# Kernel tuning notes

Hardware: AMD Instinct MI355X
Metric: run time of the kernel (lower is better)

The kernel has to match this reference:

```python
import jax, jax.numpy as jnp
import numpy as np
from jax import lax

W = 65536  # wavelength batch
L = 64     # number of stacked layers
N_IN = 1.0
N_OUT = 1.45
PURITY = 0.87
CD_SCALE = 32980.0  # mdeg conversion, as in source
LN10 = 2.302585092994046


def setup_inputs() -> dict:
    key = jax.random.key(0)
    ks = jax.random.split(key, 9)
    wl = jnp.linspace(0.4, 0.8, W, dtype=jnp.float32)  # microns, matches wl_range*1e-6 usage
    thickP = jax.random.normal(ks[0], (L,), jnp.float32) * 2.0

    def u(k, lo, hi):
        return lo + (hi - lo) * jax.random.uniform(k, (W, L), jnp.float32)

    return {
        "wl": wl,
        "thickP": thickP,
        "mind": jnp.float32(20.0),   # nm
        "maxd": jnp.float32(300.0),  # nm
        "eps_c_re": u(ks[1], 1.8, 4.5),
        "eps_c_im": u(ks[2], 0.0, 0.08),
        "kappa_c_re": u(ks[3], -5e-3, 5e-3),
        "kappa_c_im": u(ks[4], -5e-3, 5e-3),
        "eps_a_re": u(ks[5], 1.8, 4.5),
        "eps_a_im": u(ks[6], 0.0, 0.08),
        "kappa_a_re": u(ks[7], -5e-3, 5e-3),
        "kappa_a_im": u(ks[8], -5e-3, 5e-3),
    }


def _chain(Ms):
    # Ms: [L, W, 2, 2] complex; sequential layer chain-multiply (TMM recursion)
    eye = jnp.broadcast_to(jnp.eye(2, dtype=Ms.dtype), (Ms.shape[1], 2, 2))

    def step(carry, Ml):
        return jnp.einsum('wij,wjk->wik', carry, Ml), None

    Mt, _ = lax.scan(step, eye, Ms)
    return Mt  # [W, 2, 2]


def _absorbance(eps, kappa, sigma, k0, d):
    # Circular eigenmode TMM for Pasteur (isotropic chiral) layers at normal incidence.
    # eps, kappa: [W, L] complex relative quantities; k0: [W]; d: [L] meters.
    n0 = jnp.sqrt(eps)                       # background index, also wave admittance
    n_sig = n0 + sigma * kappa               # circular eigenmode index n +/- kappa
    delta = k0[:, None] * n_sig * d[None, :]  # [W, L] phase thickness
    c = jnp.cos(delta)
    s = jnp.sin(delta)
    Y = n0
    # characteristic matrix per layer: [[cos d, i sin d / Y], [i Y sin d, cos d]]
    M = jnp.stack([jnp.stack([c, 1j * s / Y], axis=-1),
                   jnp.stack([1j * Y * s, c], axis=-1)], axis=-2)  # [W, L, 2, 2]
    Mt = _chain(jnp.transpose(M, (1, 0, 2, 3)))
    m00, m01 = Mt[:, 0, 0], Mt[:, 0, 1]
    m10, m11 = Mt[:, 1, 0], Mt[:, 1, 1]
    denom = N_IN * (m00 + m01 * N_OUT) + (m10 + m11 * N_OUT)
    t = 2.0 * N_IN / denom
    T = (N_OUT / N_IN) * (jnp.abs(t) ** 2)
    return -jnp.log(T + 1e-12) / LN10  # absorbance per handedness


def _stack_cd_abs(eps_re, eps_im, kap_re, kap_im, k0, d):
    eps = (eps_re + 1j * eps_im).astype(jnp.complex64)
    kap = (kap_re + 1j * kap_im).astype(jnp.complex64)
    A_r = _absorbance(eps, kap, +1.0, k0, d)  # RCP
    A_l = _absorbance(eps, kap, -1.0, k0, d)  # LCP
    return A_l - A_r, 0.5 * (A_l + A_r)


def reference(wl, thickP, mind, maxd, eps_c_re, eps_c_im, kappa_c_re, kappa_c_im,
              eps_a_re, eps_a_im, kappa_a_re, kappa_a_im):
    d = (jax.nn.sigmoid(thickP) * (maxd - mind) + mind) * 1e-9  # [L] meters
    k0 = (2.0 * np.float32(3.1415926)) / (wl * 1e-6)             # [W]
    cd_c, abs_c = _stack_cd_abs(eps_c_re, eps_c_im, kappa_c_re, kappa_c_im, k0, d)
    cd_a, abs_a = _stack_cd_abs(eps_a_re, eps_a_im, kappa_a_re, kappa_a_im, k0, d)
    scale = (2.0 * PURITY - 1.0) * CD_SCALE
    return (cd_c * scale, cd_a * scale, abs_c, abs_a)
```

## Files before the change

kernel.cpp:

```cpp
#include <hip/hip_runtime.h>
#include <math.h>

typedef float f32x2 __attribute__((ext_vector_type(2)));

#define LTOT 64
#define GL   16
#define LPL  4

#define INV2PI  0.15915494309189535f
#define LOG2E   1.4426950408889634f
#define LOG10_2 0.30102999566398120f

struct C2 { f32x2 r, i; };
struct M2 { C2 A, B, C, D; };

__device__ __forceinline__ f32x2 shx(f32x2 v, int m) {
    f32x2 r;
    r.x = __shfl_xor(v.x, m);
    r.y = __shfl_xor(v.y, m);
    return r;
}

__device__ __forceinline__ void layer_stack(M2& M, bool first, float kd,
                                            float er, float ei, float kr, float ki) {
    float h2  = fmaf(er, er, ei * ei);
    float inv = __builtin_amdgcn_rsqf(h2);
    float mm  = h2 * inv;
    float x   = 0.5f * (mm + er);
    float rx  = __builtin_amdgcn_rsqf(x);
    float n0r = x * rx;
    float n0i = 0.5f * ei * rx;

    float ar = kd * n0r, ai = kd * n0i;
    float br = kd * kr,  bi = kd * ki;

    float rf = __builtin_amdgcn_fractf(ar * INV2PI);
    float sa = __builtin_amdgcn_sinf(rf);
    float ca = __builtin_amdgcn_cosf(rf);
    float b2 = br * br;
    float sb = br * fmaf(b2, -0.16666667f, 1.0f);
    float cb = fmaf(b2, -0.5f, 1.0f);
    float u = sa * cb, v = ca * sb, wq = ca * cb, zq = sa * sb;

    f32x2 S, Cx, Y;
    S.x = u + v;   S.y = u - v;
    Cx.x = wq - zq; Cx.y = wq + zq;
    Y.x = ai + bi; Y.y = ai - bi;

    f32x2 y2 = Y * Y;
    f32x2 ch = (y2 * 0.041666667f + 0.5f) * y2 + 1.0f;
    f32x2 sh = Y * ((y2 * 0.0083333333f + 0.16666667f) * y2 + 1.0f);

    f32x2 c_r = Cx * ch;
    f32x2 c_i = -(S * sh);
    f32x2 s_r = S * ch;
    f32x2 s_i = Cx * sh;

    f32x2 q_r = (s_r * n0r + s_i * n0i) * inv;
    f32x2 q_i = (s_i * n0r - s_r * n0i) * inv;
    f32x2 p_r = s_r * n0r - s_i * n0i;
    f32x2 p_i = s_i * n0r + s_r * n0i;

    if (first) {
        M.A.r = c_r; M.A.i = c_i;
        M.B.r = q_r; M.B.i = q_i;
        M.C.r = p_r; M.C.i = p_i;
        M.D.r = c_r; M.D.i = c_i;
    } else {
        f32x2 nAr = M.A.r*c_r - M.A.i*c_i - M.B.r*p_r + M.B.i*p_i;
        f32x2 nAi = M.A.r*c_i + M.A.i*c_r - M.B.r*p_i - M.B.i*p_r;
        f32x2 nBr = M.A.r*q_r - M.A.i*q_i + M.B.r*c_r - M.B.i*c_i;
        f32x2 nBi = M.A.r*q_i + M.A.i*q_r + M.B.r*c_i + M.B.i*c_r;
        f32x2 nCr = M.C.r*c_r - M.C.i*c_i + M.D.r*p_r - M.D.i*p_i;
        f32x2 nCi = M.C.r*c_i + M.C.i*c_r + M.D.r*p_i + M.D.i*p_r;
        f32x2 nDr = M.D.r*c_r - M.D.i*c_i - M.C.r*q_r + M.C.i*q_i;
        f32x2 nDi = M.D.r*c_i + M.D.i*c_r - M.C.r*q_i - M.C.i*q_r;
        M.A.r = nAr; M.A.i = nAi; M.B.r = nBr; M.B.i = nBi;
        M.C.r = nCr; M.C.i = nCi; M.D.r = nDr; M.D.i = nDi;
    }
}

__device__ __forceinline__ void combine(M2& L, const M2& R) {
    f32x2 nAr = L.A.r*R.A.r - L.A.i*R.A.i - L.B.r*R.C.r + L.B.i*R.C.i;
    f32x2 nAi = L.A.r*R.A.i + L.A.i*R.A.r - L.B.r*R.C.i - L.B.i*R.C.r;
    f32x2 nBr = L.A.r*R.B.r - L.A.i*R.B.i + L.B.r*R.D.r - L.B.i*R.D.i;
    f32x2 nBi = L.A.r*R.B.i + L.A.i*R.B.r + L.B.r*R.D.i + L.B.i*R.D.r;
    f32x2 nCr = L.C.r*R.A.r - L.C.i*R.A.i + L.D.r*R.C.r - L.D.i*R.C.i;
    f32x2 nCi = L.C.r*R.A.i + L.C.i*R.A.r + L.D.r*R.C.i + L.D.i*R.C.r;
    f32x2 nDr = L.D.r*R.D.r - L.D.i*R.D.i - L.C.r*R.B.r + L.C.i*R.B.i;
    f32x2 nDi = L.D.r*R.D.i + L.D.i*R.D.r - L.C.r*R.B.i - L.C.i*R.B.r;
    L.A.r = nAr; L.A.i = nAi; L.B.r = nBr; L.B.i = nBi;
    L.C.r = nCr; L.C.i = nCi; L.D.r = nDr; L.D.i = nDi;
}

__device__ __forceinline__ M2 shfl_m2(const M2& M, int m) {
    M2 R;
    R.A.r = shx(M.A.r, m); R.A.i = shx(M.A.i, m);
    R.B.r = shx(M.B.r, m); R.B.i = shx(M.B.i, m);
    R.C.r = shx(M.C.r, m); R.C.i = shx(M.C.i, m);
    R.D.r = shx(M.D.r, m); R.D.i = shx(M.D.i, m);
    return R;
}

__global__ __launch_bounds__(256, 4) void chiral_kernel(
    const float* __restrict__ wl,  const float* __restrict__ thickP,
    const float* __restrict__ mindp, const float* __restrict__ maxdp,
    const float* __restrict__ ecr, const float* __restrict__ eci,
    const float* __restrict__ kcr, const float* __restrict__ kci,
    const float* __restrict__ ear, const float* __restrict__ eai,
    const float* __restrict__ kar, const float* __restrict__ kai,
    float* __restrict__ out, int W)
{
    int t = blockIdx.x * blockDim.x + threadIdx.x;
    int w = t >> 4;
    int j = t & 15;
    if (w >= W) return;

    size_t base = (size_t)w * LTOT + (size_t)(LPL * j);

    float4 Ltp  = *reinterpret_cast<const float4*>(thickP + LPL * j);
    float4 Lecr = *reinterpret_cast<const float4*>(ecr + base);
    float4 Leci = *reinterpret_cast<const float4*>(eci + base);
    float4 Lkcr = *reinterpret_cast<const float4*>(kcr + base);
    float4 Lkci = *reinterpret_cast<const float4*>(kci + base);
    float4 Lear = *reinterpret_cast<const float4*>(ear + base);
    float4 Leai = *reinterpret_cast<const float4*>(eai + base);
    float4 Lkar = *reinterpret_cast<const float4*>(kar + base);
    float4 Lkai = *reinterpret_cast<const float4*>(kai + base);

    float lo = mindp[0], hi = maxdp[0];
    float k0 = 6.2831852e6f * __builtin_amdgcn_rcpf(wl[w]);

    const float* ptp  = reinterpret_cast<const float*>(&Ltp);
    const float* pecr = reinterpret_cast<const float*>(&Lecr);
    const float* peci = reinterpret_cast<const float*>(&Leci);
    const float* pkcr = reinterpret_cast<const float*>(&Lkcr);
    const float* pkci = reinterpret_cast<const float*>(&Lkci);
    const float* pear = reinterpret_cast<const float*>(&Lear);
    const float* peai = reinterpret_cast<const float*>(&Leai);
    const float* pkar = reinterpret_cast<const float*>(&Lkar);
    const float* pkai = reinterpret_cast<const float*>(&Lkai);

    M2 Mc, Ma;

    #pragma unroll
    for (int q = 0; q < LPL; q++) {
        bool first = (q == 0);
        float tr = ptp[q];
        float sg = __builtin_amdgcn_rcpf(1.0f + __builtin_amdgcn_exp2f(-tr * LOG2E));
        float d  = fmaf(sg, (hi - lo), lo) * 1e-9f;
        float kd = k0 * d;

        layer_stack(Mc, first, kd, pecr[q], peci[q], pkcr[q], pkci[q]);
        layer_stack(Ma, first, kd, pear[q], peai[q], pkar[q], pkai[q]);
    }

    #pragma unroll
    for (int m = 1; m < GL; m <<= 1) {
        M2 Oc = shfl_m2(Mc, m);
        M2 Oa = shfl_m2(Ma, m);
        combine(Mc, Oc);
        combine(Ma, Oa);
    }

    if (j == 0) {
        const float NOUT = 1.45f;
        f32x2 drc = Mc.A.r + NOUT * Mc.D.r - NOUT * Mc.B.i - Mc.C.i;
        f32x2 dic = Mc.A.i + NOUT * Mc.D.i + NOUT * Mc.B.r + Mc.C.r;
        f32x2 dra = Ma.A.r + NOUT * Ma.D.r - NOUT * Ma.B.i - Ma.C.i;
        f32x2 dia = Ma.A.i + NOUT * Ma.D.i + NOUT * Ma.B.r + Ma.C.r;
        f32x2 denc = drc * drc + dic * dic;
        f32x2 dena = dra * dra + dia * dia;
        float Arc = -LOG10_2 * __builtin_amdgcn_logf(5.8f * __builtin_amdgcn_rcpf(denc.x) + 1e-12f);
        float Alc = -LOG10_2 * __builtin_amdgcn_logf(5.8f * __builtin_amdgcn_rcpf(denc.y) + 1e-12f);
        float Ara = -LOG10_2 * __builtin_amdgcn_logf(5.8f * __builtin_amdgcn_rcpf(dena.x) + 1e-12f);
        float Ala = -LOG10_2 * __builtin_amdgcn_logf(5.8f * __builtin_amdgcn_rcpf(dena.y) + 1e-12f);

        const float SC = (2.0f * 0.87f - 1.0f) * 32980.0f;
        out[0 * W + w] = (Alc - Arc) * SC;
        out[1 * W + w] = (Ala - Ara) * SC;
        out[2 * W + w] = 0.5f * (Alc + Arc);
        out[3 * W + w] = 0.5f * (Ala + Ara);
    }
}

extern "C" void kernel_launch(void* const* d_in, const int* in_sizes, int n_in,
                              void* d_out, int out_size, void* d_ws, size_t ws_size,
                              hipStream_t stream) {
    const float* wl     = (const float*)d_in[0];
    const float* thickP = (const float*)d_in[1];
    const float* mind   = (const float*)d_in[2];
    const float* maxd   = (const float*)d_in[3];
    const float* ecr    = (const float*)d_in[4];
    const float* eci    = (const float*)d_in[5];
    const float* kcr    = (const float*)d_in[6];
    const float* kci    = (const float*)d_in[7];
    const float* ear    = (const float*)d_in[8];
    const float* eai    = (const float*)d_in[9];
    const float* kar    = (const float*)d_in[10];
    const float* kai    = (const float*)d_in[11];
    float* out = (float*)d_out;

    int W = in_sizes[0];
    int threads = W * GL;
    int block = 256;
    int grid = (threads + block - 1) / block;
    chiral_kernel<<<grid, block, 0, stream>>>(wl, thickP, mind, maxd,
                                              ecr, eci, kcr, kci,
                                              ear, eai, kar, kai, out, W);
}
```

Baseline: 173.7 us.

## Process two wavelengths per thread group with software-prefetched second load

Each 16-lane group now handles two wavelengths (w and w+W/2), halving the grid. The second wavelength's eight float4 loads are issued before the first wavelength's layer math, with sched_barriers to keep that order, so memory latency overlaps compute. The per-layer thickness sigmoid is computed once and reused for both wavelengths. This costs extra registers (32 more floats live), which may reduce occupancy, and it assumes an even W.

```diff
diff --git a/kernel.cpp b/kernel.cpp
--- a/kernel.cpp
+++ b/kernel.cpp
@@ -13,6 +13,10 @@
 
 struct C2 { f32x2 r, i; };
 struct M2 { C2 A, B, C, D; };
+struct Regs {
+    float4 ecr, eci, kcr, kci, ear, eai, kar, kai;
+    float k0;
+};
 
 __device__ __forceinline__ f32x2 shx(f32x2 v, int m) {
     f32x2 r;
@@ -102,59 +106,49 @@
     return R;
 }
 
-__global__ __launch_bounds__(256, 4) void chiral_kernel(
-    const float* __restrict__ wl,  const float* __restrict__ thickP,
-    const float* __restrict__ mindp, const float* __restrict__ maxdp,
+__device__ __forceinline__ Regs load_all(
+    const float* __restrict__ wl,
     const float* __restrict__ ecr, const float* __restrict__ eci,
     const float* __restrict__ kcr, const float* __restrict__ kci,
     const float* __restrict__ ear, const float* __restrict__ eai,
     const float* __restrict__ kar, const float* __restrict__ kai,
-    float* __restrict__ out, int W)
-{
-    int t = blockIdx.x * blockDim.x + threadIdx.x;
-    int w = t >> 4;
-    int j = t & 15;
-    if (w >= W) return;
-
-    size_t base = (size_t)w * LTOT + (size_t)(LPL * j);
-
-    float4 Ltp  = *reinterpret_cast<const float4*>(thickP + LPL * j);
-    float4 Lecr = *reinterpret_cast<const float4*>(ecr + base);
-    float4 Leci = *reinterpret_cast<const float4*>(eci + base);
-    float4 Lkcr = *reinterpret_cast<const float4*>(kcr + base);
-    float4 Lkci = *reinterpret_cast<const float4*>(kci + base);
-    float4 Lear = *reinterpret_cast<const float4*>(ear + base);
-    float4 Leai = *reinterpret_cast<const float4*>(eai + base);
-    float4 Lkar = *reinterpret_cast<const float4*>(kar + base);
-    float4 Lkai = *reinterpret_cast<const float4*>(kai + base);
-
-    float lo = mindp[0], hi = maxdp[0];
-    float k0 = 6.2831852e6f * __builtin_amdgcn_rcpf(wl[w]);
-
-    const float* ptp  = reinterpret_cast<const float*>(&Ltp);
-    const float* pecr = reinterpret_cast<const float*>(&Lecr);
-    const float* peci = reinterpret_cast<const float*>(&Leci);
-    const float* pkcr = reinterpret_cast<const float*>(&Lkcr);
-    const float* pkci = reinterpret_cast<const float*>(&Lkci);
-    const float* pear = reinterpret_cast<const float*>(&Lear);
-    const float* peai = reinterpret_cast<const float*>(&Leai);
-    const float* pkar = reinterpret_cast<const float*>(&Lkar);
-    const float* pkai = reinterpret_cast<const float*>(&Lkai);
-
-    M2 Mc, Ma;
-
+    size_t base, int w)
+{
+    Regs R;
+    R.ecr = *reinterpret_cast<const float4*>(ecr + base);
+    R.eci = *reinterpret_cast<const float4*>(eci + base);
+    R.kcr = *reinterpret_cast<const float4*>(kcr + base);
+    R.kci = *reinterpret_cast<const float4*>(kci + base);
+    R.ear = *reinterpret_cast<const float4*>(ear + base);
+    R.eai = *reinterpret_cast<const float4*>(eai + base);
+    R.kar = *reinterpret_cast<const float4*>(kar + base);
+    R.kai = *reinterpret_cast<const float4*>(kai + base);
+    R.k0  = 6.2831852e6f * __builtin_amdgcn_rcpf(wl[w]);
+    return R;
+}
+
+__device__ __forceinline__ void layers(const Regs& R, const float* dq, M2& Mc, M2& Ma)
+{
+    const float* pecr = reinterpret_cast<const float*>(&R.ecr);
+    const float* peci = reinterpret_cast<const float*>(&R.eci);
+    const float* pkcr = reinterpret_cast<const float*>(&R.kcr);
+    const float* pkci = reinterpret_cast<const float*>(&R.kci);
+    const float* pear = reinterpret_cast<const float*>(&R.ear);
+    const float* peai = reinterpret_cast<const float*>(&R.eai);
+    const float* pkar = reinterpret_cast<const float*>(&R.kar);
+    const float* pkai = reinterpret_cast<const float*>(&R.kai);
     #pragma unroll
     for (int q = 0; q < LPL; q++) {
         bool first = (q == 0);
-        float tr = ptp[q];
-        float sg = __builtin_amdgcn_rcpf(1.0f + __builtin_amdgcn_exp2f(-tr * LOG2E));
-        float d  = fmaf(sg, (hi - lo), lo) * 1e-9f;
-        float kd = k0 * d;
-
+        float kd = R.k0 * dq[q];
         layer_stack(Mc, first, kd, pecr[q], peci[q], pkcr[q], pkci[q]);
         layer_stack(Ma, first, kd, pear[q], peai[q], pkar[q], pkai[q]);
     }
-
+}
+
+__device__ __forceinline__ void reduce_store(M2 Mc, M2 Ma, int j, int w, int W,
+                                             float* __restrict__ out)
+{
     #pragma unroll
     for (int m = 1; m < GL; m <<= 1) {
         M2 Oc = shfl_m2(Mc, m);
@@ -182,6 +176,49 @@
         out[2 * W + w] = 0.5f * (Alc + Arc);
         out[3 * W + w] = 0.5f * (Ala + Ara);
     }
+}
+
+__global__ __launch_bounds__(256, 4) void chiral_kernel(
+    const float* __restrict__ wl,  const float* __restrict__ thickP,
+    const float* __restrict__ mindp, const float* __restrict__ maxdp,
+    const float* __restrict__ ecr, const float* __restrict__ eci,
+    const float* __restrict__ kcr, const float* __restrict__ kci,
+    const float* __restrict__ ear, const float* __restrict__ eai,
+    const float* __restrict__ kar, const float* __restrict__ kai,
+    float* __restrict__ out, int W)
+{
+    int t  = blockIdx.x * blockDim.x + threadIdx.x;
+    int Wh = W >> 1;
+    int w0 = t >> 4;
+    int j  = t & 15;
+    if (w0 >= Wh) return;
+    int w1 = w0 + Wh;
+
+    size_t b0 = (size_t)w0 * LTOT + (size_t)(LPL * j);
+    size_t b1 = (size_t)w1 * LTOT + (size_t)(LPL * j);
+
+    Regs R0 = load_all(wl, ecr, eci, kcr, kci, ear, eai, kar, kai, b0, w0);
+
+    float lo = mindp[0], hi = maxdp[0];
+    float4 tp4 = *reinterpret_cast<const float4*>(thickP + LPL * j);
+    const float* ptp = reinterpret_cast<const float*>(&tp4);
+    float dq[LPL];
+    #pragma unroll
+    for (int q = 0; q < LPL; q++) {
+        float sg = __builtin_amdgcn_rcpf(1.0f + __builtin_amdgcn_exp2f(-ptp[q] * LOG2E));
+        dq[q] = fmaf(sg, hi - lo, lo) * 1e-9f;
+    }
+    __builtin_amdgcn_sched_barrier(0);
+
+    Regs R1 = load_all(wl, ecr, eci, kcr, kci, ear, eai, kar, kai, b1, w1);
+    M2 Mc0, Ma0;
+    layers(R0, dq, Mc0, Ma0);
+    __builtin_amdgcn_sched_barrier(0);
+
+    reduce_store(Mc0, Ma0, j, w0, W, out);
+    M2 Mc1, Ma1;
+    layers(R1, dq, Mc1, Ma1);
+    reduce_store(Mc1, Ma1, j, w1, W, out);
 }
 
 extern "C" void kernel_launch(void* const* d_in, const int* in_sizes, int n_in,
@@ -202,7 +239,7 @@
     float* out = (float*)d_out;
 
     int W = in_sizes[0];
-    int threads = W * GL;
+    int threads = (W / 2) * GL;
     int block = 256;
     int grid = (threads + block - 1) / block;
     chiral_kernel<<<grid, block, 0, stream>>>(wl, thickP, mind, maxd,
```

New measurement: 174.0 us. About the same (+0.2%).

## Make waves persistent over several wavelength tiles with double-buffered async LDS loads

Applied to the files above, without the earlier changes.

Each wave now handles four groups of four wavelengths. The next group's eight input arrays are prefetched into a double-buffered LDS region with global_load_lds while the current group is computed. The per-layer thickness and sigmoid are computed once per wave and reused across iterations, and the grid shrinks accordingly. The aim is to hide global memory latency behind the TMM math. The cost is 64KB of LDS per block and a lower occupancy hint, so fewer waves are resident to hide latency.

```diff
diff --git a/kernel.cpp b/kernel.cpp
--- a/kernel.cpp
+++ b/kernel.cpp
@@ -1,11 +1,13 @@
 #include <hip/hip_runtime.h>
 #include <math.h>
+#include <stdint.h>
 
 typedef float f32x2 __attribute__((ext_vector_type(2)));
 
 #define LTOT 64
 #define GL   16
 #define LPL  4
+#define NT   4
 
 #define INV2PI  0.15915494309189535f
 #define LOG2E   1.4426950408889634f
@@ -13,6 +15,9 @@
 
 struct C2 { f32x2 r, i; };
 struct M2 { C2 A, B, C, D; };
+
+typedef __attribute__((address_space(3))) uint32_t lds_u32;
+typedef __attribute__((address_space(1))) const uint32_t gbl_u32;
 
 __device__ __forceinline__ f32x2 shx(f32x2 v, int m) {
     f32x2 r;
@@ -102,7 +107,7 @@
     return R;
 }
 
-__global__ __launch_bounds__(256, 4) void chiral_kernel(
+__global__ __launch_bounds__(256, 2) void chiral_kernel(
     const float* __restrict__ wl,  const float* __restrict__ thickP,
     const float* __restrict__ mindp, const float* __restrict__ maxdp,
     const float* __restrict__ ecr, const float* __restrict__ eci,
@@ -111,77 +116,116 @@
     const float* __restrict__ kar, const float* __restrict__ kai,
     float* __restrict__ out, int W)
 {
-    int t = blockIdx.x * blockDim.x + threadIdx.x;
-    int w = t >> 4;
-    int j = t & 15;
-    if (w >= W) return;
-
-    size_t base = (size_t)w * LTOT + (size_t)(LPL * j);
-
-    float4 Ltp  = *reinterpret_cast<const float4*>(thickP + LPL * j);
-    float4 Lecr = *reinterpret_cast<const float4*>(ecr + base);
-    float4 Leci = *reinterpret_cast<const float4*>(eci + base);
-    float4 Lkcr = *reinterpret_cast<const float4*>(kcr + base);
-    float4 Lkci = *reinterpret_cast<const float4*>(kci + base);
-    float4 Lear = *reinterpret_cast<const float4*>(ear + base);
-    float4 Leai = *reinterpret_cast<const float4*>(eai + base);
-    float4 Lkar = *reinterpret_cast<const float4*>(kar + base);
-    float4 Lkai = *reinterpret_cast<const float4*>(kai + base);
-
-    float lo = mindp[0], hi = maxdp[0];
-    float k0 = 6.2831852e6f * __builtin_amdgcn_rcpf(wl[w]);
-
-    const float* ptp  = reinterpret_cast<const float*>(&Ltp);
-    const float* pecr = reinterpret_cast<const float*>(&Lecr);
-    const float* peci = reinterpret_cast<const float*>(&Leci);
-    const float* pkcr = reinterpret_cast<const float*>(&Lkcr);
-    const float* pkci = reinterpret_cast<const float*>(&Lkci);
-    const float* pear = reinterpret_cast<const float*>(&Lear);
-    const float* peai = reinterpret_cast<const float*>(&Leai);
-    const float* pkar = reinterpret_cast<const float*>(&Lkar);
-    const float* pkai = reinterpret_cast<const float*>(&Lkai);
-
-    M2 Mc, Ma;
-
+    __shared__ float lds[4][2][8][256];
+
+    const int tid  = threadIdx.x;
+    const int v    = tid >> 6;
+    const int lane = tid & 63;
+    const int grp  = lane >> 4;
+    const int j    = lane & 15;
+
+    const int wavegid = blockIdx.x * 4 + v;
+    const int w0 = wavegid * (4 * NT);
+    if (w0 >= W) return;
+
+    const size_t laneoff = (size_t)grp * LTOT + 4 * (size_t)j;
+
+#define STAGE(buf, wbase) do {                                                            \
+        size_t g_ = (size_t)(wbase) * LTOT + laneoff;                                     \
+        float* dst_ = &lds[v][(buf)][0][0];                                               \
+        __builtin_amdgcn_global_load_lds((gbl_u32*)(ecr + g_), (lds_u32*)(dst_ + 0*256), 16, 0, 0); \
+        __builtin_amdgcn_global_load_lds((gbl_u32*)(eci + g_), (lds_u32*)(dst_ + 1*256), 16, 0, 0); \
+        __builtin_amdgcn_global_load_lds((gbl_u32*)(kcr + g_), (lds_u32*)(dst_ + 2*256), 16, 0, 0); \
+        __builtin_amdgcn_global_load_lds((gbl_u32*)(kci + g_), (lds_u32*)(dst_ + 3*256), 16, 0, 0); \
+        __builtin_amdgcn_global_load_lds((gbl_u32*)(ear + g_), (lds_u32*)(dst_ + 4*256), 16, 0, 0); \
+        __builtin_amdgcn_global_load_lds((gbl_u32*)(eai + g_), (lds_u32*)(dst_ + 5*256), 16, 0, 0); \
+        __builtin_amdgcn_global_load_lds((gbl_u32*)(kar + g_), (lds_u32*)(dst_ + 6*256), 16, 0, 0); \
+        __builtin_amdgcn_global_load_lds((gbl_u32*)(kai + g_), (lds_u32*)(dst_ + 7*256), 16, 0, 0); \
+    } while (0)
+
+    STAGE(0, w0);
+    float wlv = wl[w0 + grp];
+
+    const float lo = mindp[0], hi = maxdp[0];
+    float4 tp4 = *reinterpret_cast<const float4*>(thickP + LPL * j);
+    const float* ptp = reinterpret_cast<const float*>(&tp4);
+    float dq[LPL];
     #pragma unroll
     for (int q = 0; q < LPL; q++) {
-        bool first = (q == 0);
-        float tr = ptp[q];
-        float sg = __builtin_amdgcn_rcpf(1.0f + __builtin_amdgcn_exp2f(-tr * LOG2E));
-        float d  = fmaf(sg, (hi - lo), lo) * 1e-9f;
-        float kd = k0 * d;
-
-        layer_stack(Mc, first, kd, pecr[q], peci[q], pkcr[q], pkci[q]);
-        layer_stack(Ma, first, kd, pear[q], peai[q], pkar[q], pkai[q]);
+        float sg = __builtin_amdgcn_rcpf(1.0f + __builtin_amdgcn_exp2f(-ptp[q] * LOG2E));
+        dq[q] = fmaf(sg, hi - lo, lo) * 1e-9f;
     }
 
     #pragma unroll
-    for (int m = 1; m < GL; m <<= 1) {
-        M2 Oc = shfl_m2(Mc, m);
-        M2 Oa = shfl_m2(Ma, m);
-        combine(Mc, Oc);
-        combine(Ma, Oa);
+    for (int t = 0; t < NT; t++) {
+        const int cur = t & 1;
+        const int w = w0 + 4 * t + grp;
+        float k0 = 6.2831852e6f * __builtin_amdgcn_rcpf(wlv);
+
+        asm volatile("s_waitcnt vmcnt(0)" ::: "memory");
+        __builtin_amdgcn_sched_barrier(0);
+        const float* wb = &lds[v][cur][0][0];
+        float4 Decr = *reinterpret_cast<const float4*>(wb + 0*256 + 4*lane);
+        float4 Deci = *reinterpret_cast<const float4*>(wb + 1*256 + 4*lane);
+        float4 Dkcr = *reinterpret_cast<const float4*>(wb + 2*256 + 4*lane);
+        float4 Dkci = *reinterpret_cast<const float4*>(wb + 3*256 + 4*lane);
+        float4 Dear = *reinterpret_cast<const float4*>(wb + 4*256 + 4*lane);
+        float4 Deai = *reinterpret_cast<const float4*>(wb + 5*256 + 4*lane);
+        float4 Dkar = *reinterpret_cast<const float4*>(wb + 6*256 + 4*lane);
+        float4 Dkai = *reinterpret_cast<const float4*>(wb + 7*256 + 4*lane);
+
+        if (t + 1 < NT) {
+            STAGE(cur ^ 1, w0 + 4 * (t + 1));
+            wlv = wl[w0 + 4 * (t + 1) + grp];
+        }
+
+        const float* pecr = reinterpret_cast<const float*>(&Decr);
+        const float* peci = reinterpret_cast<const float*>(&Deci);
+        const float* pkcr = reinterpret_cast<const float*>(&Dkcr);
+        const float* pkci = reinterpret_cast<const float*>(&Dkci);
+        const float* pear = reinterpret_cast<const float*>(&Dear);
+        const float* peai = reinterpret_cast<const float*>(&Deai);
+        const float* pkar = reinterpret_cast<const float*>(&Dkar);
+        const float* pkai = reinterpret_cast<const float*>(&Dkai);
+
+        M2 Mc, Ma;
+        #pragma unroll
+        for (int q = 0; q < LPL; q++) {
+            bool first = (q == 0);
+            float kd = k0 * dq[q];
+            layer_stack(Mc, first, kd, pecr[q], peci[q], pkcr[q], pkci[q]);
+            layer_stack(Ma, first, kd, pear[q], peai[q], pkar[q], pkai[q]);
+        }
+
+        #pragma unroll
+        for (int m = 1; m < GL; m <<= 1) {
+            M2 Oc = shfl_m2(Mc, m);
+            M2 Oa = shfl_m2(Ma, m);
+            combine(Mc, Oc);
+            combine(Ma, Oa);
+        }
+
+        if (j == 0 && w < W) {
+            const float NOUT = 1.45f;
+            f32x2 drc = Mc.A.r + NOUT * Mc.D.r - NOUT * Mc.B.i - Mc.C.i;
+            f32x2 dic = Mc.A.i + NOUT * Mc.D.i + NOUT * Mc.B.r + Mc.C.r;
+            f32x2 dra = Ma.A.r + NOUT * Ma.D.r - NOUT * Ma.B.i - Ma.C.i;
+            f32x2 dia = Ma.A.i + NOUT * Ma.D.i + NOUT * Ma.B.r + Ma.C.r;
+            f32x2 denc = drc * drc + dic * dic;
+            f32x2 dena = dra * dra + dia * dia;
+            float Arc = -LOG10_2 * __builtin_amdgcn_logf(5.8f * __builtin_amdgcn_rcpf(denc.x) + 1e-12f);
+            float Alc = -LOG10_2 * __builtin_amdgcn_logf(5.8f * __builtin_amdgcn_rcpf(denc.y) + 1e-12f);
+            float Ara = -LOG10_2 * __builtin_amdgcn_logf(5.8f * __builtin_amdgcn_rcpf(dena.x) + 1e-12f);
+            float Ala = -LOG10_2 * __builtin_amdgcn_logf(5.8f * __builtin_amdgcn_rcpf(dena.y) + 1e-12f);
+
+            const float SC = (2.0f * 0.87f - 1.0f) * 32980.0f;
+            out[0 * W + w] = (Alc - Arc) * SC;
+            out[1 * W + w] = (Ala - Ara) * SC;
+            out[2 * W + w] = 0.5f * (Alc + Arc);
+            out[3 * W + w] = 0.5f * (Ala + Ara);
+        }
     }
-
-    if (j == 0) {
-        const float NOUT = 1.45f;
-        f32x2 drc = Mc.A.r + NOUT * Mc.D.r - NOUT * Mc.B.i - Mc.C.i;
-        f32x2 dic = Mc.A.i + NOUT * Mc.D.i + NOUT * Mc.B.r + Mc.C.r;
-        f32x2 dra = Ma.A.r + NOUT * Ma.D.r - NOUT * Ma.B.i - Ma.C.i;
-        f32x2 dia = Ma.A.i + NOUT * Ma.D.i + NOUT * Ma.B.r + Ma.C.r;
-        f32x2 denc = drc * drc + dic * dic;
-        f32x2 dena = dra * dra + dia * dia;
-        float Arc = -LOG10_2 * __builtin_amdgcn_logf(5.8f * __builtin_amdgcn_rcpf(denc.x) + 1e-12f);
-        float Alc = -LOG10_2 * __builtin_amdgcn_logf(5.8f * __builtin_amdgcn_rcpf(denc.y) + 1e-12f);
-        float Ara = -LOG10_2 * __builtin_amdgcn_logf(5.8f * __builtin_amdgcn_rcpf(dena.x) + 1e-12f);
-        float Ala = -LOG10_2 * __builtin_amdgcn_logf(5.8f * __builtin_amdgcn_rcpf(dena.y) + 1e-12f);
-
-        const float SC = (2.0f * 0.87f - 1.0f) * 32980.0f;
-        out[0 * W + w] = (Alc - Arc) * SC;
-        out[1 * W + w] = (Ala - Ara) * SC;
-        out[2 * W + w] = 0.5f * (Alc + Arc);
-        out[3 * W + w] = 0.5f * (Ala + Ara);
-    }
+#undef STAGE
 }
 
 extern "C" void kernel_launch(void* const* d_in, const int* in_sizes, int n_in,
@@ -202,10 +246,9 @@
     float* out = (float*)d_out;
 
     int W = in_sizes[0];
-    int threads = W * GL;
-    int block = 256;
-    int grid = (threads + block - 1) / block;
-    chiral_kernel<<<grid, block, 0, stream>>>(wl, thickP, mind, maxd,
-                                              ecr, eci, kcr, kci,
-                                              ear, eai, kar, kai, out, W);
-}
+    int wl_per_block = 4 * NT * 4;
+    int grid = (W + wl_per_block - 1) / wl_per_block;
+    chiral_kernel<<<grid, 256, 0, stream>>>(wl, thickP, mind, maxd,
+                                            ecr, eci, kcr, kci,
+                                            ear, eai, kar, kai, out, W);
+}
```

Result: slower. 184.3 us (+6.1%).

## Process two wavelengths per 16-lane group with 4-wide vector math

Applied to the files above, without the earlier changes.

Each 16-lane group now handles two adjacent wavelengths, widening the per-thread matrix state from 2-wide to 4-wide vectors. Layer thickness/sigmoid work is computed once and shared across both wavelengths. The shuffle-based tree reduction count per wavelength is halved relative to lanes, and the grid shrinks by half. This doubles register pressure (launch bounds lowered to 2 blocks/SM) and assumes W is even.

```diff
diff --git a/kernel.cpp b/kernel.cpp
--- a/kernel.cpp
+++ b/kernel.cpp
@@ -1,7 +1,7 @@
 #include <hip/hip_runtime.h>
 #include <math.h>
 
-typedef float f32x2 __attribute__((ext_vector_type(2)));
+typedef float f32x4 __attribute__((ext_vector_type(4)));
 
 #define LTOT 64
 #define GL   16
@@ -11,55 +11,73 @@
 #define LOG2E   1.4426950408889634f
 #define LOG10_2 0.30102999566398120f
 
-struct C2 { f32x2 r, i; };
-struct M2 { C2 A, B, C, D; };
-
-__device__ __forceinline__ f32x2 shx(f32x2 v, int m) {
-    f32x2 r;
-    r.x = __shfl_xor(v.x, m);
-    r.y = __shfl_xor(v.y, m);
+struct C4 { f32x4 r, i; };
+struct M4 { C4 A, B, C, D; };
+
+__device__ __forceinline__ f32x4 shx4(f32x4 v, int m) {
+    f32x4 r;
+    r.x = __shfl_xor(v.x, m); r.y = __shfl_xor(v.y, m);
+    r.z = __shfl_xor(v.z, m); r.w = __shfl_xor(v.w, m);
     return r;
 }
 
-__device__ __forceinline__ void layer_stack(M2& M, bool first, float kd,
-                                            float er, float ei, float kr, float ki) {
-    float h2  = fmaf(er, er, ei * ei);
-    float inv = __builtin_amdgcn_rsqf(h2);
-    float mm  = h2 * inv;
-    float x   = 0.5f * (mm + er);
-    float rx  = __builtin_amdgcn_rsqf(x);
-    float n0r = x * rx;
-    float n0i = 0.5f * ei * rx;
-
-    float ar = kd * n0r, ai = kd * n0i;
-    float br = kd * kr,  bi = kd * ki;
-
-    float rf = __builtin_amdgcn_fractf(ar * INV2PI);
-    float sa = __builtin_amdgcn_sinf(rf);
-    float ca = __builtin_amdgcn_cosf(rf);
-    float b2 = br * br;
-    float sb = br * fmaf(b2, -0.16666667f, 1.0f);
-    float cb = fmaf(b2, -0.5f, 1.0f);
-    float u = sa * cb, v = ca * sb, wq = ca * cb, zq = sa * sb;
-
-    f32x2 S, Cx, Y;
-    S.x = u + v;   S.y = u - v;
-    Cx.x = wq - zq; Cx.y = wq + zq;
-    Y.x = ai + bi; Y.y = ai - bi;
-
-    f32x2 y2 = Y * Y;
-    f32x2 ch = (y2 * 0.041666667f + 0.5f) * y2 + 1.0f;
-    f32x2 sh = Y * ((y2 * 0.0083333333f + 0.16666667f) * y2 + 1.0f);
-
-    f32x2 c_r = Cx * ch;
-    f32x2 c_i = -(S * sh);
-    f32x2 s_r = S * ch;
-    f32x2 s_i = Cx * sh;
-
-    f32x2 q_r = (s_r * n0r + s_i * n0i) * inv;
-    f32x2 q_i = (s_i * n0r - s_r * n0i) * inv;
-    f32x2 p_r = s_r * n0r - s_i * n0i;
-    f32x2 p_i = s_i * n0r + s_r * n0i;
+__device__ __forceinline__ void layer2(M4& M, bool first,
+    float kd0, float kd1,
+    float er0, float ei0, float kr0, float ki0,
+    float er1, float ei1, float kr1, float ki1)
+{
+    float h20 = fmaf(er0, er0, ei0 * ei0);
+    float iv0 = __builtin_amdgcn_rsqf(h20);
+    float mm0 = h20 * iv0;
+    float x0  = 0.5f * (mm0 + er0);
+    float rx0 = __builtin_amdgcn_rsqf(x0);
+    float n0r0 = x0 * rx0, n0i0 = 0.5f * ei0 * rx0;
+    float ar0 = kd0 * n0r0, ai0 = kd0 * n0i0;
+    float br0 = kd0 * kr0,  bi0 = kd0 * ki0;
+    float rf0 = __builtin_amdgcn_fractf(ar0 * INV2PI);
+    float sa0 = __builtin_amdgcn_sinf(rf0);
+    float ca0 = __builtin_amdgcn_cosf(rf0);
+    float b20 = br0 * br0;
+    float sb0 = br0 * fmaf(b20, -0.16666667f, 1.0f);
+    float cb0 = fmaf(b20, -0.5f, 1.0f);
+    float u0 = sa0 * cb0, v0 = ca0 * sb0, cc0 = ca0 * cb0, zz0 = sa0 * sb0;
+
+    float h21 = fmaf(er1, er1, ei1 * ei1);
+    float iv1 = __builtin_amdgcn_rsqf(h21);
+    float mm1 = h21 * iv1;
+    float x1  = 0.5f * (mm1 + er1);
+    float rx1 = __builtin_amdgcn_rsqf(x1);
+    float n0r1 = x1 * rx1, n0i1 = 0.5f * ei1 * rx1;
+    float ar1 = kd1 * n0r1, ai1 = kd1 * n0i1;
+    float br1 = kd1 * kr1,  bi1 = kd1 * ki1;
+    float rf1 = __builtin_amdgcn_fractf(ar1 * INV2PI);
+    float sa1 = __builtin_amdgcn_sinf(rf1);
+    float ca1 = __builtin_amdgcn_cosf(rf1);
+    float b21 = br1 * br1;
+    float sb1 = br1 * fmaf(b21, -0.16666667f, 1.0f);
+    float cb1 = fmaf(b21, -0.5f, 1.0f);
+    float u1 = sa1 * cb1, v1 = ca1 * sb1, cc1 = ca1 * cb1, zz1 = sa1 * sb1;
+
+    f32x4 S  = { u0 + v0,  u0 - v0,  u1 + v1,  u1 - v1  };
+    f32x4 Cx = { cc0 - zz0, cc0 + zz0, cc1 - zz1, cc1 + zz1 };
+    f32x4 Y  = { ai0 + bi0, ai0 - bi0, ai1 + bi1, ai1 - bi1 };
+    f32x4 Nr = { n0r0, n0r0, n0r1, n0r1 };
+    f32x4 Ni = { n0i0, n0i0, n0i1, n0i1 };
+    f32x4 IV = { iv0, iv0, iv1, iv1 };
+
+    f32x4 y2 = Y * Y;
+    f32x4 ch = (y2 * 0.041666667f + 0.5f) * y2 + 1.0f;
+    f32x4 sh = Y * ((y2 * 0.0083333333f + 0.16666667f) * y2 + 1.0f);
+
+    f32x4 c_r = Cx * ch;
+    f32x4 c_i = -(S * sh);
+    f32x4 s_r = S * ch;
+    f32x4 s_i = Cx * sh;
+
+    f32x4 q_r = (s_r * Nr + s_i * Ni) * IV;
+    f32x4 q_i = (s_i * Nr - s_r * Ni) * IV;
+    f32x4 p_r = s_r * Nr - s_i * Ni;
+    f32x4 p_i = s_i * Nr + s_r * Ni;
 
     if (first) {
         M.A.r = c_r; M.A.i = c_i;
@@ -67,42 +85,42 @@
         M.C.r = p_r; M.C.i = p_i;
         M.D.r = c_r; M.D.i = c_i;
     } else {
-        f32x2 nAr = M.A.r*c_r - M.A.i*c_i - M.B.r*p_r + M.B.i*p_i;
-        f32x2 nAi = M.A.r*c_i + M.A.i*c_r - M.B.r*p_i - M.B.i*p_r;
-        f32x2 nBr = M.A.r*q_r - M.A.i*q_i + M.B.r*c_r - M.B.i*c_i;
-        f32x2 nBi = M.A.r*q_i + M.A.i*q_r + M.B.r*c_i + M.B.i*c_r;
-        f32x2 nCr = M.C.r*c_r - M.C.i*c_i + M.D.r*p_r - M.D.i*p_i;
-        f32x2 nCi = M.C.r*c_i + M.C.i*c_r + M.D.r*p_i + M.D.i*p_r;
-        f32x2 nDr = M.D.r*c_r - M.D.i*c_i - M.C.r*q_r + M.C.i*q_i;
-        f32x2 nDi = M.D.r*c_i + M.D.i*c_r - M.C.r*q_i - M.C.i*q_r;
+        f32x4 nAr = M.A.r*c_r - M.A.i*c_i - M.B.r*p_r + M.B.i*p_i;
+        f32x4 nAi = M.A.r*c_i + M.A.i*c_r - M.B.r*p_i - M.B.i*p_r;
+        f32x4 nBr = M.A.r*q_r - M.A.i*q_i + M.B.r*c_r - M.B.i*c_i;
+        f32x4 nBi = M.A.r*q_i + M.A.i*q_r + M.B.r*c_i + M.B.i*c_r;
+        f32x4 nCr = M.C.r*c_r - M.C.i*c_i + M.D.r*p_r - M.D.i*p_i;
+        f32x4 nCi = M.C.r*c_i + M.C.i*c_r + M.D.r*p_i + M.D.i*p_r;
+        f32x4 nDr = M.D.r*c_r - M.D.i*c_i - M.C.r*q_r + M.C.i*q_i;
+        f32x4 nDi = M.D.r*c_i + M.D.i*c_r - M.C.r*q_i - M.C.i*q_r;
         M.A.r = nAr; M.A.i = nAi; M.B.r = nBr; M.B.i = nBi;
         M.C.r = nCr; M.C.i = nCi; M.D.r = nDr; M.D.i = nDi;
     }
 }
 
-__device__ __forceinline__ void combine(M2& L, const M2& R) {
-    f32x2 nAr = L.A.r*R.A.r - L.A.i*R.A.i - L.B.r*R.C.r + L.B.i*R.C.i;
-    f32x2 nAi = L.A.r*R.A.i + L.A.i*R.A.r - L.B.r*R.C.i - L.B.i*R.C.r;
-    f32x2 nBr = L.A.r*R.B.r - L.A.i*R.B.i + L.B.r*R.D.r - L.B.i*R.D.i;
-    f32x2 nBi = L.A.r*R.B.i + L.A.i*R.B.r + L.B.r*R.D.i + L.B.i*R.D.r;
-    f32x2 nCr = L.C.r*R.A.r - L.C.i*R.A.i + L.D.r*R.C.r - L.D.i*R.C.i;
-    f32x2 nCi = L.C.r*R.A.i + L.C.i*R.A.r + L.D.r*R.C.i + L.D.i*R.C.r;
-    f32x2 nDr = L.D.r*R.D.r - L.D.i*R.D.i - L.C.r*R.B.r + L.C.i*R.B.i;
-    f32x2 nDi = L.D.r*R.D.i + L.D.i*R.D.r - L.C.r*R.B.i - L.C.i*R.B.r;
+__device__ __forceinline__ void combine4(M4& L, const M4& R) {
+    f32x4 nAr = L.A.r*R.A.r - L.A.i*R.A.i - L.B.r*R.C.r + L.B.i*R.C.i;
+    f32x4 nAi = L.A.r*R.A.i + L.A.i*R.A.r - L.B.r*R.C.i - L.B.i*R.C.r;
+    f32x4 nBr = L.A.r*R.B.r - L.A.i*R.B.i + L.B.r*R.D.r - L.B.i*R.D.i;
+    f32x4 nBi = L.A.r*R.B.i + L.A.i*R.B.r + L.B.r*R.D.i + L.B.i*R.D.r;
+    f32x4 nCr = L.C.r*R.A.r - L.C.i*R.A.i + L.D.r*R.C.r - L.D.i*R.C.i;
+    f32x4 nCi = L.C.r*R.A.i + L.C.i*R.A.r + L.D.r*R.C.i + L.D.i*R.C.r;
+    f32x4 nDr = L.D.r*R.D.r - L.D.i*R.D.i - L.C.r*R.B.r + L.C.i*R.B.i;
+    f32x4 nDi = L.D.r*R.D.i + L.D.i*R.D.r - L.C.r*R.B.i - L.C.i*R.B.r;
     L.A.r = nAr; L.A.i = nAi; L.B.r = nBr; L.B.i = nBi;
     L.C.r = nCr; L.C.i = nCi; L.D.r = nDr; L.D.i = nDi;
 }
 
-__device__ __forceinline__ M2 shfl_m2(const M2& M, int m) {
-    M2 R;
-    R.A.r = shx(M.A.r, m); R.A.i = shx(M.A.i, m);
-    R.B.r = shx(M.B.r, m); R.B.i = shx(M.B.i, m);
-    R.C.r = shx(M.C.r, m); R.C.i = shx(M.C.i, m);
-    R.D.r = shx(M.D.r, m); R.D.i = shx(M.D.i, m);
+__device__ __forceinline__ M4 shfl_m4(const M4& M, int m) {
+    M4 R;
+    R.A.r = shx4(M.A.r, m); R.A.i = shx4(M.A.i, m);
+    R.B.r = shx4(M.B.r, m); R.B.i = shx4(M.B.i, m);
+    R.C.r = shx4(M.C.r, m); R.C.i = shx4(M.C.i, m);
+    R.D.r = shx4(M.D.r, m); R.D.i = shx4(M.D.i, m);
     return R;
 }
 
-__global__ __launch_bounds__(256, 4) void chiral_kernel(
+__global__ __launch_bounds__(256, 2) void chiral_kernel(
     const float* __restrict__ wl,  const float* __restrict__ thickP,
     const float* __restrict__ mindp, const float* __restrict__ maxdp,
     const float* __restrict__ ecr, const float* __restrict__ eci,
@@ -112,75 +130,107 @@
     float* __restrict__ out, int W)
 {
     int t = blockIdx.x * blockDim.x + threadIdx.x;
-    int w = t >> 4;
+    int g = t >> 4;
     int j = t & 15;
-    if (w >= W) return;
-
-    size_t base = (size_t)w * LTOT + (size_t)(LPL * j);
-
-    float4 Ltp  = *reinterpret_cast<const float4*>(thickP + LPL * j);
-    float4 Lecr = *reinterpret_cast<const float4*>(ecr + base);
-    float4 Leci = *reinterpret_cast<const float4*>(eci + base);
-    float4 Lkcr = *reinterpret_cast<const float4*>(kcr + base);
-    float4 Lkci = *reinterpret_cast<const float4*>(kci + base);
-    float4 Lear = *reinterpret_cast<const float4*>(ear + base);
-    float4 Leai = *reinterpret_cast<const float4*>(eai + base);
-    float4 Lkar = *reinterpret_cast<const float4*>(kar + base);
-    float4 Lkai = *reinterpret_cast<const float4*>(kai + base);
+    if (g >= (W >> 1)) return;
+    int w0 = 2 * g, w1 = w0 + 1;
+
+    size_t b0 = (size_t)w0 * LTOT + (size_t)(LPL * j);
+    size_t b1 = b0 + LTOT;
+
+    float4 Ltp   = *reinterpret_cast<const float4*>(thickP + LPL * j);
+    float4 Lecr0 = *reinterpret_cast<const float4*>(ecr + b0);
+    float4 Leci0 = *reinterpret_cast<const float4*>(eci + b0);
+    float4 Lkcr0 = *reinterpret_cast<const float4*>(kcr + b0);
+    float4 Lkci0 = *reinterpret_cast<const float4*>(kci + b0);
+    float4 Lear0 = *reinterpret_cast<const float4*>(ear + b0);
+    float4 Leai0 = *reinterpret_cast<const float4*>(eai + b0);
+    float4 Lkar0 = *reinterpret_cast<const float4*>(kar + b0);
+    float4 Lkai0 = *reinterpret_cast<const float4*>(kai + b0);
+    float4 Lecr1 = *reinterpret_cast<const float4*>(ecr + b1);
+    float4 Leci1 = *reinterpret_cast<const float4*>(eci + b1);
+    float4 Lkcr1 = *reinterpret_cast<const float4*>(kcr + b1);
+    float4 Lkci1 = *reinterpret_cast<const float4*>(kci + b1);
+    float4 Lear1 = *reinterpret_cast<const float4*>(ear + b1);
+    float4 Leai1 = *reinterpret_cast<const float4*>(eai + b1);
+    float4 Lkar1 = *reinterpret_cast<const float4*>(kar + b1);
+    float4 Lkai1 = *reinterpret_cast<const float4*>(kai + b1);
 
     float lo = mindp[0], hi = maxdp[0];
-    float k0 = 6.2831852e6f * __builtin_amdgcn_rcpf(wl[w]);
-
-    const float* ptp  = reinterpret_cast<const float*>(&Ltp);
-    const float* pecr = reinterpret_cast<const float*>(&Lecr);
-    const float* peci = reinterpret_cast<const float*>(&Leci);
-    const float* pkcr = reinterpret_cast<const float*>(&Lkcr);
-    const float* pkci = reinterpret_cast<const float*>(&Lkci);
-    const float* pear = reinterpret_cast<const float*>(&Lear);
-    const float* peai = reinterpret_cast<const float*>(&Leai);
-    const float* pkar = reinterpret_cast<const float*>(&Lkar);
-    const float* pkai = reinterpret_cast<const float*>(&Lkai);
-
-    M2 Mc, Ma;
+    float k00 = 6.2831852e6f * __builtin_amdgcn_rcpf(wl[w0]);
+    float k01 = 6.2831852e6f * __builtin_amdgcn_rcpf(wl[w1]);
+
+    const float* ptp = reinterpret_cast<const float*>(&Ltp);
+    float dq[LPL];
+    #pragma unroll
+    for (int q = 0; q < LPL; q++) {
+        float sg = __builtin_amdgcn_rcpf(1.0f + __builtin_amdgcn_exp2f(-ptp[q] * LOG2E));
+        dq[q] = fmaf(sg, hi - lo, lo) * 1e-9f;
+    }
+
+    const float* pecr0 = reinterpret_cast<const float*>(&Lecr0);
+    const float* peci0 = reinterpret_cast<const float*>(&Leci0);
+    const float* pkcr0 = reinterpret_cast<const float*>(&Lkcr0);
+    const float* pkci0 = reinterpret_cast<const float*>(&Lkci0);
+    const float* pear0 = reinterpret_cast<const float*>(&Lear0);
+    const float* peai0 = reinterpret_cast<const float*>(&Leai0);
+    const float* pkar0 = reinterpret_cast<const float*>(&Lkar0);
+    const float* pkai0 = reinterpret_cast<const float*>(&Lkai0);
+    const float* pecr1 = reinterpret_cast<const float*>(&Lecr1);
+    const float* peci1 = reinterpret_cast<const float*>(&Leci1);
+    const float* pkcr1 = reinterpret_cast<const float*>(&Lkcr1);
+    const float* pkci1 = reinterpret_cast<const float*>(&Lkci1);
+    const float* pear1 = reinterpret_cast<const float*>(&Lear1);
+    const float* peai1 = reinterpret_cast<const float*>(&Leai1);
+    const float* pkar1 = reinterpret_cast<const float*>(&Lkar1);
+    const float* pkai1 = reinterpret_cast<const float*>(&Lkai1);
+
+    M4 Mc, Ma;
 
     #pragma unroll
     for (int q = 0; q < LPL; q++) {
         bool first = (q == 0);
-        float tr = ptp[q];
-        float sg = __builtin_amdgcn_rcpf(1.0f + __builtin_amdgcn_exp2f(-tr * LOG2E));
-        float d  = fmaf(sg, (hi - lo), lo) * 1e-9f;
-        float kd = k0 * d;
-
-        layer_stack(Mc, first, kd, pecr[q], peci[q], pkcr[q], pkci[q]);
-        layer_stack(Ma, first, kd, pear[q], peai[q], pkar[q], pkai[q]);
+        float kd0 = k00 * dq[q];
+        float kd1 = k01 * dq[q];
+        layer2(Mc, first, kd0, kd1,
+               pecr0[q], peci0[q], pkcr0[q], pkci0[q],
+               pecr1[q], peci1[q], pkcr1[q], pkci1[q]);
+        layer2(Ma, first, kd0, kd1,
+               pear0[q], peai0[q], pkar0[q], pkai0[q],
+               pear1[q], peai1[q], pkar1[q], pkai1[q]);
     }
 
     #pragma unroll
     for (int m = 1; m < GL; m <<= 1) {
-        M2 Oc = shfl_m2(Mc, m);
-        M2 Oa = shfl_m2(Ma, m);
-        combine(Mc, Oc);
-        combine(Ma, Oa);
+        M4 Oc = shfl_m4(Mc, m);
+        combine4(Mc, Oc);
+        M4 Oa = shfl_m4(Ma, m);
+        combine4(Ma, Oa);
     }
 
     if (j == 0) {
         const float NOUT = 1.45f;
-        f32x2 drc = Mc.A.r + NOUT * Mc.D.r - NOUT * Mc.B.i - Mc.C.i;
-        f32x2 dic = Mc.A.i + NOUT * Mc.D.i + NOUT * Mc.B.r + Mc.C.r;
-        f32x2 dra = Ma.A.r + NOUT * Ma.D.r - NOUT * Ma.B.i - Ma.C.i;
-        f32x2 dia = Ma.A.i + NOUT * Ma.D.i + NOUT * Ma.B.r + Ma.C.r;
-        f32x2 denc = drc * drc + dic * dic;
-        f32x2 dena = dra * dra + dia * dia;
-        float Arc = -LOG10_2 * __builtin_amdgcn_logf(5.8f * __builtin_amdgcn_rcpf(denc.x) + 1e-12f);
-        float Alc = -LOG10_2 * __builtin_amdgcn_logf(5.8f * __builtin_amdgcn_rcpf(denc.y) + 1e-12f);
-        float Ara = -LOG10_2 * __builtin_amdgcn_logf(5.8f * __builtin_amdgcn_rcpf(dena.x) + 1e-12f);
-        float Ala = -LOG10_2 * __builtin_amdgcn_logf(5.8f * __builtin_amdgcn_rcpf(dena.y) + 1e-12f);
-
+        f32x4 drc = Mc.A.r + NOUT * Mc.D.r - NOUT * Mc.B.i - Mc.C.i;
+        f32x4 dic = Mc.A.i + NOUT * Mc.D.i + NOUT * Mc.B.r + Mc.C.r;
+        f32x4 dra = Ma.A.r + NOUT * Ma.D.r - NOUT * Ma.B.i - Ma.C.i;
+        f32x4 dia = Ma.A.i + NOUT * Ma.D.i + NOUT * Ma.B.r + Ma.C.r;
+        f32x4 denc = drc * drc + dic * dic;
+        f32x4 dena = dra * dra + dia * dia;
+#define ALOG(d) (-LOG10_2 * __builtin_amdgcn_logf(5.8f * __builtin_amdgcn_rcpf(d) + 1e-12f))
+        float Arc0 = ALOG(denc.x), Alc0 = ALOG(denc.y);
+        float Arc1 = ALOG(denc.z), Alc1 = ALOG(denc.w);
+        float Ara0 = ALOG(dena.x), Ala0 = ALOG(dena.y);
+        float Ara1 = ALOG(dena.z), Ala1 = ALOG(dena.w);
+#undef ALOG
         const float SC = (2.0f * 0.87f - 1.0f) * 32980.0f;
-        out[0 * W + w] = (Alc - Arc) * SC;
-        out[1 * W + w] = (Ala - Ara) * SC;
-        out[2 * W + w] = 0.5f * (Alc + Arc);
-        out[3 * W + w] = 0.5f * (Ala + Ara);
+        out[0 * W + w0] = (Alc0 - Arc0) * SC;
+        out[0 * W + w1] = (Alc1 - Arc1) * SC;
+        out[1 * W + w0] = (Ala0 - Ara0) * SC;
+        out[1 * W + w1] = (Ala1 - Ara1) * SC;
+        out[2 * W + w0] = 0.5f * (Alc0 + Arc0);
+        out[2 * W + w1] = 0.5f * (Alc1 + Arc1);
+        out[3 * W + w0] = 0.5f * (Ala0 + Ara0);
+        out[3 * W + w1] = 0.5f * (Ala1 + Ara1);
     }
 }
 
@@ -202,9 +252,9 @@
     float* out = (float*)d_out;
 
     int W = in_sizes[0];
-    int threads = W * GL;
+    long long threads = (long long)(W / 2) * GL;
     int block = 256;
-    int grid = (threads + block - 1) / block;
+    int grid = (int)((threads + block - 1) / block);
     chiral_kernel<<<grid, block, 0, stream>>>(wl, thickP, mind, maxd,
                                               ecr, eci, kcr, kci,
                                               ear, eai, kar, kai, out, W);
```

New measurement: 180.2 us. +3.7%, slower.
